# Kernel tuning notes

Hardware: AMD Instinct MI355X
Metric: run time of the kernel (lower is better)

Reference implementation:

```python
import jax, jax.numpy as jnp
import numpy as np

D_MODEL = 1024
N_HEADS = 16
D_K = D_MODEL // N_HEADS
MAX_SEQ = 2048
THETA = 10000.0


def _make_cos_sin():
    # cos_sin[i, k, 0] = cos(i / theta**(2k/d_k)), [.., 1] = sin(...)
    pos = np.arange(MAX_SEQ, dtype=np.float32)[:, None]
    k = np.arange(D_K // 2, dtype=np.float32)[None, :]
    ang = pos / (THETA ** (2.0 * k / D_K))
    return jnp.asarray(np.stack([np.cos(ang), np.sin(ang)], axis=-1), dtype=jnp.float32)


def setup_inputs() -> dict:
    key = jax.random.key(0)
    ks = jax.random.split(key, 5)
    std = 2.0 / (D_MODEL + D_MODEL)
    def w(k):
        return std * jax.random.truncated_normal(k, -3.0, 3.0, (D_MODEL, D_MODEL), dtype=jnp.float32)
    return {
        "x": jax.random.normal(ks[0], (4, 2048, D_MODEL), dtype=jnp.float32),
        "Wq": w(ks[1]),
        "Wk": w(ks[2]),
        "Wv": w(ks[3]),
        "Wo": w(ks[4]),
        "cos_sin": _make_cos_sin(),
        "token_positions": jnp.arange(2048, dtype=jnp.int32),
    }


def _rope(x, cos_sin, pos):
    # x: [B, H, S, d_k]; rotate consecutive pairs
    B, H, S, d = x.shape
    xt = x.reshape(B, H, S, d // 2, 2)
    cos = cos_sin[pos, :, 0]  # [S, d/2]
    sin = cos_sin[pos, :, 1]
    x0, x1 = xt[..., 0], xt[..., 1]
    r0 = cos * x0 - sin * x1
    r1 = sin * x0 + cos * x1
    return jnp.stack([r0, r1], axis=-1).reshape(B, H, S, d)


def reference(x, Wq, Wk, Wv, Wo, cos_sin, token_positions):
    B, S, D = x.shape
    H, d = N_HEADS, D_K
    def proj(W):
        y = jnp.einsum('bsi,oi->bso', x, W)
        return y.reshape(B, S, H, d).transpose(0, 2, 1, 3)  # [B,H,S,d]
    q = _rope(proj(Wq), cos_sin, token_positions)
    k = _rope(proj(Wk), cos_sin, token_positions)
    v = proj(Wv)
    scores = jnp.einsum('bhqd,bhkd->bhqk', q, k) / jnp.sqrt(jnp.float32(d))
    causal = jnp.tril(jnp.ones((S, S), dtype=bool))
    scores = jnp.where(causal, scores, -jnp.inf)
    attn = jax.nn.softmax(scores, axis=-1)
    out = jnp.einsum('bhqk,bhkd->bhqd', attn, v)
    out = out.transpose(0, 2, 1, 3).reshape(B, S, D)
    return jnp.einsum('bsi,oi->bso', out, Wo)
```

## Files before the change

kernel.cpp:

```cpp
#include <hip/hip_runtime.h>

constexpr int B_  = 4;
constexpr int S_  = 2048;
constexpr int D_  = 1024;
constexpr int H_  = 16;
constexpr int DK_ = 64;
constexpr int M_  = B_ * S_;

typedef __attribute__((ext_vector_type(8))) short short8;
typedef __attribute__((ext_vector_type(4))) float f32x4;
typedef __attribute__((ext_vector_type(4))) unsigned short us4;
typedef __attribute__((ext_vector_type(4))) unsigned int u32x4;

__device__ __forceinline__ unsigned short f2b(float f) {
  unsigned int u = __float_as_uint(f);
  u += 0x7FFFu + ((u >> 16) & 1u);
  return (unsigned short)(u >> 16);
}
__device__ __forceinline__ float b2f(unsigned short h) {
  return __uint_as_float(((unsigned int)h) << 16);
}
__device__ __forceinline__ unsigned int cvtpk(float lo, float hi) {
  unsigned int w;
  asm("v_cvt_pk_bf16_f32 %0, %1, %2" : "=v"(w) : "v"(lo), "v"(hi));
  return w;
}
__device__ __forceinline__ float exp2v(float x) {
  float r;
  asm("v_exp_f32 %0, %1" : "=v"(r) : "v"(x));
  return r;
}

#define GLOAD16(g, l) __builtin_amdgcn_global_load_lds( \
    (const __attribute__((address_space(1))) unsigned int*)(g), \
    (__attribute__((address_space(3))) unsigned int*)(l), 16, 0, 0)

__global__ __launch_bounds__(256) void conv_kernel(
    const float* __restrict__ x,
    const float* __restrict__ wq, const float* __restrict__ wk, const float* __restrict__ wv,
    unsigned short* __restrict__ xb, unsigned short* __restrict__ wb)
{
  const int NX4 = (M_ * D_) / 4;
  const int NW4 = (3 * D_ * D_) / 4;
  int stride = gridDim.x * blockDim.x;
  for (int i = blockIdx.x * blockDim.x + threadIdx.x; i < NX4 + NW4; i += stride) {
    const float4* src; unsigned short* dst; int o;
    if (i < NX4) { src = (const float4*)x; dst = xb; o = i; }
    else {
      int wi = i - NX4;
      int mat = wi >> 18;
      o = wi & 262143;
      src = (const float4*)(mat == 0 ? wq : (mat == 1 ? wk : wv));
      dst = wb + mat * (D_ * D_);
    }
    float4 v = src[o];
    us4 r; r.x = f2b(v.x); r.y = f2b(v.y); r.z = f2b(v.z); r.w = f2b(v.w);
    *(us4*)(dst + o * 4) = r;
  }
}

__global__ __launch_bounds__(256) void conv_wo_kernel(
    const float* __restrict__ wo, unsigned short* __restrict__ wob)
{
  int i = blockIdx.x * 256 + threadIdx.x;
  float4 v = ((const float4*)wo)[i];
  us4 r; r.x = f2b(v.x); r.y = f2b(v.y); r.z = f2b(v.z); r.w = f2b(v.w);
  *(us4*)(wob + i * 4) = r;
}

__global__ __launch_bounds__(256, 2) void gemm_qkv_kernel(
    const unsigned short* __restrict__ xb,
    const unsigned short* __restrict__ wb,
    const float* __restrict__ cs,
    const int* __restrict__ pos,
    unsigned short* __restrict__ qb,
    unsigned short* __restrict__ kb,
    unsigned short* __restrict__ vtb)
{
  __shared__ unsigned short As[2][128 * 64];
  __shared__ unsigned short Bs[2][128 * 64];
  const int tid  = threadIdx.x;
  const int lane = tid & 63;
  const int wid  = tid >> 6;
  const int wm = wid >> 1, wn = wid & 1;
  const int m0 = blockIdx.x * 128;
  const int n0 = blockIdx.y * 128;
  const int l15 = lane & 15, l4 = lane >> 4;
  const int swz7 = l15 & 7;

  int srow[4], sgcc[4], slds[4];
  #pragma unroll
  for (int j = 0; j < 4; ++j) {
    int c = tid + j * 256;
    srow[j] = c >> 3;
    int cc  = c & 7;
    sgcc[j] = cc ^ (srow[j] & 7);
    slds[j] = (wid * 64 + j * 256) * 8;
  }

  f32x4 acc[4][4] = {};

  #pragma unroll
  for (int j = 0; j < 4; ++j) {
    GLOAD16(xb + (m0 + srow[j]) * D_ + sgcc[j] * 8, &As[0][slds[j]]);
    GLOAD16(wb + (n0 + srow[j]) * D_ + sgcc[j] * 8, &Bs[0][slds[j]]);
  }
  __syncthreads();

  for (int t = 0; t < 16; ++t) {
    const int cur = t & 1, nxt = cur ^ 1;
    if (t < 15) {
      const int kcol = (t + 1) * 64;
      #pragma unroll
      for (int j = 0; j < 4; ++j) {
        GLOAD16(xb + (m0 + srow[j]) * D_ + kcol + sgcc[j] * 8, &As[nxt][slds[j]]);
        GLOAD16(wb + (n0 + srow[j]) * D_ + kcol + sgcc[j] * 8, &Bs[nxt][slds[j]]);
      }
    }
    const unsigned short* Ab = &As[cur][0];
    const unsigned short* Bb = &Bs[cur][0];
    #pragma unroll
    for (int ks = 0; ks < 2; ++ks) {
      const int cc = (ks * 4 + l4) ^ swz7;
      short8 af[4], bfr[4];
      #pragma unroll
      for (int mi = 0; mi < 4; ++mi) af[mi]  = *(const short8*)&Ab[(wm*64 + mi*16 + l15)*64 + cc*8];
      #pragma unroll
      for (int ni = 0; ni < 4; ++ni) bfr[ni] = *(const short8*)&Bb[(wn*64 + ni*16 + l15)*64 + cc*8];
      __builtin_amdgcn_s_setprio(1);
      #pragma unroll
      for (int mi = 0; mi < 4; ++mi)
        #pragma unroll
        for (int ni = 0; ni < 4; ++ni)
          acc[mi][ni] = __builtin_amdgcn_mfma_f32_16x16x32_bf16(af[mi], bfr[ni], acc[mi][ni], 0, 0, 0);
      __builtin_amdgcn_s_setprio(0);
    }
    __syncthreads();
  }

  const int bidx = m0 >> 11;
  const int sbase = (m0 & 2047) + wm * 64;

  if (n0 < 2048) {
    unsigned short* dst = (n0 < 1024) ? qb : kb;
    const int nn0 = n0 & 1023;
    const float2* cs2 = (const float2*)cs;
    const float sg = (l15 & 1) ? 1.0f : -1.0f;
    #pragma unroll
    for (int mi = 0; mi < 4; ++mi)
      #pragma unroll
      for (int j = 0; j < 4; ++j) {
        int s = sbase + mi*16 + l4*4 + j;
        int p = pos[s];
        #pragma unroll
        for (int ni = 0; ni < 4; ++ni) {
          int col = nn0 + wn*64 + ni*16 + l15;
          int h = col >> 6, dd = col & 63;
          float val = acc[mi][ni][j];
          float par = __shfl_xor(val, 1);
          float2 cv = cs2[p*32 + (dd >> 1)];
          float r = fmaf(cv.x, val, sg * cv.y * par);
          dst[((bidx*H_ + h)*S_ + s)*DK_ + dd] = f2b(r);
        }
      }
  } else {
    const int nn0 = n0 & 1023;
    const int hB = (nn0 + wn*64) >> 6;
    #pragma unroll
    for (int mi = 0; mi < 4; ++mi) {
      int s4 = sbase + mi*16 + l4*4;
      int a  = s4 >> 2, bgr = a & 7;
      int s4p = ((a & ~7) + ((bgr & 3)*2 + (bgr >> 2))) << 2;
      #pragma unroll
      for (int ni = 0; ni < 4; ++ni) {
        int dd = ni*16 + l15;
        uint2 w;
        w.x = cvtpk(acc[mi][ni][0], acc[mi][ni][1]);
        w.y = cvtpk(acc[mi][ni][2], acc[mi][ni][3]);
        *(uint2*)(vtb + ((bidx*H_ + hB)*DK_ + dd)*S_ + s4p) = w;
      }
    }
  }
}

__global__ __launch_bounds__(256, 4) void attn_kernel(
    const unsigned short* __restrict__ qb,
    const unsigned short* __restrict__ kb,
    const unsigned short* __restrict__ vtb,
    unsigned short* __restrict__ ao)
{
  __shared__ unsigned short Ks[2][64 * 64];
  __shared__ unsigned short Vs[2][64 * 64];
  const int tid = threadIdx.x, lane = tid & 63, wid = tid >> 6;
  const int l15 = lane & 15, l4 = lane >> 4;
  const int swz7 = l15 & 7;

  const int id  = blockIdx.x;
  const int xcd = id & 7, rem = id >> 3;
  const int bh  = xcd * 8 + (rem & 7);
  const int qt  = 15 - (rem >> 3);
  const int q0  = qt * 128;
  const int nkt = 2 * qt + 2;

  const unsigned short* qp = qb  + bh * S_ * DK_;
  const unsigned short* kp = kb  + bh * S_ * DK_;
  const unsigned short* vp = vtb + bh * DK_ * S_;
  const int bidx = bh >> 4, h = bh & 15;

  int srow[2], sgcc[2], slds[2];
  #pragma unroll
  for (int j = 0; j < 2; ++j) {
    int c = tid + j * 256;
    srow[j] = c >> 3;
    int cc  = c & 7;
    sgcc[j] = cc ^ (srow[j] & 7);
    slds[j] = (wid * 64 + j * 256) * 8;
  }

  const float QSC = 0.18033688f;
  short8 qf[2][2];
  #pragma unroll
  for (int y = 0; y < 2; ++y)
    #pragma unroll
    for (int kbk = 0; kbk < 2; ++kbk) {
      short8 raw = *(const short8*)(qp + (q0 + y*64 + wid*16 + l15)*DK_ + kbk*32 + l4*8);
      #pragma unroll
      for (int i = 0; i < 8; ++i) {
        float f = b2f((unsigned short)raw[i]) * QSC;
        raw[i] = (short)f2b(f);
      }
      qf[y][kbk] = raw;
    }

  f32x4 oacc[2][4] = {};
  float mrun[2] = {-1e30f, -1e30f}, lrun[2] = {0.0f, 0.0f};

  #pragma unroll
  for (int j = 0; j < 2; ++j) {
    GLOAD16(kp + srow[j]*DK_ + sgcc[j]*8, &Ks[0][slds[j]]);
    GLOAD16(vp + srow[j]*S_  + sgcc[j]*8, &Vs[0][slds[j]]);
  }
  __syncthreads();

  for (int kt = 0; kt < nkt; ++kt) {
    const int cur = kt & 1, nxt = cur ^ 1;
    if (kt + 1 < nkt) {
      const int kb0 = (kt + 1) * 64;
      #pragma unroll
      for (int j = 0; j < 2; ++j) {
        GLOAD16(kp + (kb0 + srow[j])*DK_ + sgcc[j]*8, &Ks[nxt][slds[j]]);
        GLOAD16(vp + srow[j]*S_ + kb0   + sgcc[j]*8, &Vs[nxt][slds[j]]);
      }
    }

    #pragma unroll
    for (int y = 0; y < 2; ++y) {
      if (kt > 2*qt + y) continue;

      f32x4 sc[4];
      __builtin_amdgcn_s_setprio(1);
      #pragma unroll
      for (int nb = 0; nb < 4; ++nb) {
        const int rb = (nb*16 + l15) * 64;
        short8 k0 = *(const short8*)&Ks[cur][rb + ((l4     ^ swz7) * 8)];
        short8 k1 = *(const short8*)&Ks[cur][rb + (((4+l4) ^ swz7) * 8)];
        f32x4 z = {};
        z = __builtin_amdgcn_mfma_f32_16x16x32_bf16(k0, qf[y][0], z, 0, 0, 0);
        z = __builtin_amdgcn_mfma_f32_16x16x32_bf16(k1, qf[y][1], z, 0, 0, 0);
        sc[nb] = z;
      }
      __builtin_amdgcn_s_setprio(0);

      if (kt == 2*qt + y) {
        const int qg = q0 + y*64 + wid*16 + l15;
        #pragma unroll
        for (int nb = 0; nb < 4; ++nb)
          #pragma unroll
          for (int j = 0; j < 4; ++j) {
            int kg = kt*64 + nb*16 + l4*4 + j;
            if (kg > qg) sc[nb][j] = -1e30f;
          }
      }

      float mq[4];
      #pragma unroll
      for (int nb = 0; nb < 4; ++nb)
        mq[nb] = fmaxf(fmaxf(sc[nb][0], sc[nb][1]), fmaxf(sc[nb][2], sc[nb][3]));
      float tm = fmaxf(fmaxf(mq[0], mq[1]), fmaxf(mq[2], mq[3]));
      tm = fmaxf(tm, __shfl_xor(tm, 16));
      tm = fmaxf(tm, __shfl_xor(tm, 32));
      if (!__all(tm - mrun[y] <= 8.0f)) {
        float mnew = fmaxf(mrun[y], tm);
        float corr = exp2v(mrun[y] - mnew);
        mrun[y] = mnew;
        lrun[y] *= corr;
        #pragma unroll
        for (int nb = 0; nb < 4; ++nb)
          #pragma unroll
          for (int j = 0; j < 4; ++j) oacc[y][nb][j] *= corr;
      }
      float sq[4];
      #pragma unroll
      for (int nb = 0; nb < 4; ++nb) {
        #pragma unroll
        for (int j = 0; j < 4; ++j) sc[nb][j] = exp2v(sc[nb][j] - mrun[y]);
        sq[nb] = (sc[nb][0] + sc[nb][1]) + (sc[nb][2] + sc[nb][3]);
      }
      float rs = (sq[0] + sq[1]) + (sq[2] + sq[3]);
      rs += __shfl_xor(rs, 16);
      rs += __shfl_xor(rs, 32);
      lrun[y] += rs;

      u32x4 pa0v = { cvtpk(sc[0][0], sc[0][1]), cvtpk(sc[0][2], sc[0][3]),
                     cvtpk(sc[1][0], sc[1][1]), cvtpk(sc[1][2], sc[1][3]) };
      u32x4 pa1v = { cvtpk(sc[2][0], sc[2][1]), cvtpk(sc[2][2], sc[2][3]),
                     cvtpk(sc[3][0], sc[3][1]), cvtpk(sc[3][2], sc[3][3]) };
      short8 pa0 = __builtin_bit_cast(short8, pa0v);
      short8 pa1 = __builtin_bit_cast(short8, pa1v);

      __builtin_amdgcn_s_setprio(1);
      #pragma unroll
      for (int nb = 0; nb < 4; ++nb) {
        const int rb = (nb*16 + l15) * 64;
        short8 v0 = *(const short8*)&Vs[cur][rb + ((l4     ^ swz7) * 8)];
        short8 v1 = *(const short8*)&Vs[cur][rb + (((4+l4) ^ swz7) * 8)];
        oacc[y][nb] = __builtin_amdgcn_mfma_f32_16x16x32_bf16(v0, pa0, oacc[y][nb], 0, 0, 0);
        oacc[y][nb] = __builtin_amdgcn_mfma_f32_16x16x32_bf16(v1, pa1, oacc[y][nb], 0, 0, 0);
      }
      __builtin_amdgcn_s_setprio(0);
    }

    __syncthreads();
  }

  #pragma unroll
  for (int y = 0; y < 2; ++y) {
    float inv = 1.0f / lrun[y];
    int row = q0 + y*64 + wid*16 + l15;
    unsigned short* obase = ao + ((bidx*S_ + row)*H_ + h)*DK_;
    #pragma unroll
    for (int nb = 0; nb < 4; ++nb) {
      uint2 w;
      w.x = cvtpk(oacc[y][nb][0] * inv, oacc[y][nb][1] * inv);
      w.y = cvtpk(oacc[y][nb][2] * inv, oacc[y][nb][3] * inv);
      *(uint2*)(obase + nb*16 + l4*4) = w;
    }
  }
}

__global__ __launch_bounds__(256, 2) void gemm_out_kernel(
    const unsigned short* __restrict__ ao,
    const unsigned short* __restrict__ wob,
    float* __restrict__ out)
{
  __shared__ unsigned short As[2][128 * 64];
  __shared__ unsigned short Bs[2][128 * 64];
  const int tid = threadIdx.x, lane = tid & 63, wid = tid >> 6;
  const int wm = wid >> 1, wn = wid & 1;
  const int m0 = blockIdx.x * 128, n0 = blockIdx.y * 128;
  const int l15 = lane & 15, l4 = lane >> 4;
  const int swz7 = l15 & 7;

  int srow[4], sgcc[4], slds[4];
  #pragma unroll
  for (int j = 0; j < 4; ++j) {
    int c = tid + j * 256;
    srow[j] = c >> 3;
    int cc  = c & 7;
    sgcc[j] = cc ^ (srow[j] & 7);
    slds[j] = (wid * 64 + j * 256) * 8;
  }

  f32x4 acc[4][4] = {};

  #pragma unroll
  for (int j = 0; j < 4; ++j) {
    GLOAD16(ao  + (m0 + srow[j]) * D_ + sgcc[j] * 8, &As[0][slds[j]]);
    GLOAD16(wob + (n0 + srow[j]) * D_ + sgcc[j] * 8, &Bs[0][slds[j]]);
  }
  __syncthreads();

  for (int t = 0; t < 16; ++t) {
    const int cur = t & 1, nxt = cur ^ 1;
    if (t < 15) {
      const int kcol = (t + 1) * 64;
      #pragma unroll
      for (int j = 0; j < 4; ++j) {
        GLOAD16(ao  + (m0 + srow[j]) * D_ + kcol + sgcc[j] * 8, &As[nxt][slds[j]]);
        GLOAD16(wob + (n0 + srow[j]) * D_ + kcol + sgcc[j] * 8, &Bs[nxt][slds[j]]);
      }
    }
    const unsigned short* Ab = &As[cur][0];
    const unsigned short* Bb = &Bs[cur][0];
    #pragma unroll
    for (int ks = 0; ks < 2; ++ks) {
      const int cc = (ks * 4 + l4) ^ swz7;
      short8 af[4], bfr[4];
      #pragma unroll
      for (int mi = 0; mi < 4; ++mi) af[mi]  = *(const short8*)&Ab[(wm*64 + mi*16 + l15)*64 + cc*8];
      #pragma unroll
      for (int ni = 0; ni < 4; ++ni) bfr[ni] = *(const short8*)&Bb[(wn*64 + ni*16 + l15)*64 + cc*8];
      __builtin_amdgcn_s_setprio(1);
      #pragma unroll
      for (int mi = 0; mi < 4; ++mi)
        #pragma unroll
        for (int ni = 0; ni < 4; ++ni)
          acc[mi][ni] = __builtin_amdgcn_mfma_f32_16x16x32_bf16(af[mi], bfr[ni], acc[mi][ni], 0, 0, 0);
      __builtin_amdgcn_s_setprio(0);
    }
    __syncthreads();
  }

  #pragma unroll
  for (int mi = 0; mi < 4; ++mi)
    #pragma unroll
    for (int ni = 0; ni < 4; ++ni)
      #pragma unroll
      for (int j = 0; j < 4; ++j) {
        int row = m0 + wm*64 + mi*16 + l4*4 + j;
        int col = n0 + wn*64 + ni*16 + l15;
        out[row * D_ + col] = acc[mi][ni][j];
      }
}

extern "C" void kernel_launch(void* const* d_in, const int* in_sizes, int n_in,
                              void* d_out, int out_size, void* d_ws, size_t ws_size,
                              hipStream_t stream)
{
  const float* x  = (const float*)d_in[0];
  const float* wq = (const float*)d_in[1];
  const float* wk = (const float*)d_in[2];
  const float* wv = (const float*)d_in[3];
  const float* wo = (const float*)d_in[4];
  const float* cs = (const float*)d_in[5];
  const int*  pos = (const int*)d_in[6];
  float* out = (float*)d_out;

  unsigned short* xb = (unsigned short*)d_out;
  unsigned short* wb = xb + M_ * D_;

  unsigned short* qb  = (unsigned short*)d_ws;
  unsigned short* kbf = qb  + M_ * D_;
  unsigned short* vtb = kbf + M_ * D_;
  unsigned short* aob = vtb + M_ * D_;
  unsigned short* wob = qb;

  conv_kernel<<<dim3(2048), dim3(256), 0, stream>>>(x, wq, wk, wv, xb, wb);
  gemm_qkv_kernel<<<dim3(64, 24), dim3(256), 0, stream>>>(xb, wb, cs, pos, qb, kbf, vtb);
  attn_kernel<<<dim3(1024), dim3(256), 0, stream>>>(qb, kbf, vtb, aob);
  conv_wo_kernel<<<dim3(1024), dim3(256), 0, stream>>>(wo, wob);
  gemm_out_kernel<<<dim3(64, 8), dim3(256), 0, stream>>>(aob, wob, out);

  (void)in_sizes; (void)n_in; (void)out_size; (void)ws_size;
}
```

Measured before the change: 173.6 us.

## Replace double-buffered K=64 GEMM pipeline with single-buffer K=32 tiles

Both projection GEMMs drop the double-buffered 64-wide K staging and use a single 32-wide K tile per iteration, with two barriers around each load and a new XOR swizzle for the narrower rows. This quarters LDS use per block, which may allow more resident blocks, and simplifies the loop. The cost is that loads no longer overlap with MFMA work inside a block, and the barrier count per K element doubles.

Measured after the change: 181.4 us. 1.04x slower.

```diff
diff --git a/kernel.cpp b/kernel.cpp
--- a/kernel.cpp
+++ b/kernel.cpp
@@ -77,8 +77,8 @@
     unsigned short* __restrict__ kb,
     unsigned short* __restrict__ vtb)
 {
-  __shared__ unsigned short As[2][128 * 64];
-  __shared__ unsigned short Bs[2][128 * 64];
+  __shared__ unsigned short As[128 * 32];
+  __shared__ unsigned short Bs[128 * 32];
   const int tid  = threadIdx.x;
   const int lane = tid & 63;
   const int wid  = tid >> 6;
@@ -86,56 +86,42 @@
   const int m0 = blockIdx.x * 128;
   const int n0 = blockIdx.y * 128;
   const int l15 = lane & 15, l4 = lane >> 4;
-  const int swz7 = l15 & 7;
-
-  int srow[4], sgcc[4], slds[4];
-  #pragma unroll
-  for (int j = 0; j < 4; ++j) {
+  const int fsw = (l15 >> 1) & 3;
+
+  int srow[2], sgcc[2], slds[2];
+  #pragma unroll
+  for (int j = 0; j < 2; ++j) {
     int c = tid + j * 256;
-    srow[j] = c >> 3;
-    int cc  = c & 7;
-    sgcc[j] = cc ^ (srow[j] & 7);
+    srow[j] = c >> 2;
+    int cc  = c & 3;
+    sgcc[j] = cc ^ ((srow[j] >> 1) & 3);
     slds[j] = (wid * 64 + j * 256) * 8;
   }
 
   f32x4 acc[4][4] = {};
 
-  #pragma unroll
-  for (int j = 0; j < 4; ++j) {
-    GLOAD16(xb + (m0 + srow[j]) * D_ + sgcc[j] * 8, &As[0][slds[j]]);
-    GLOAD16(wb + (n0 + srow[j]) * D_ + sgcc[j] * 8, &Bs[0][slds[j]]);
-  }
-  __syncthreads();
-
-  for (int t = 0; t < 16; ++t) {
-    const int cur = t & 1, nxt = cur ^ 1;
-    if (t < 15) {
-      const int kcol = (t + 1) * 64;
-      #pragma unroll
-      for (int j = 0; j < 4; ++j) {
-        GLOAD16(xb + (m0 + srow[j]) * D_ + kcol + sgcc[j] * 8, &As[nxt][slds[j]]);
-        GLOAD16(wb + (n0 + srow[j]) * D_ + kcol + sgcc[j] * 8, &Bs[nxt][slds[j]]);
-      }
-    }
-    const unsigned short* Ab = &As[cur][0];
-    const unsigned short* Bb = &Bs[cur][0];
-    #pragma unroll
-    for (int ks = 0; ks < 2; ++ks) {
-      const int cc = (ks * 4 + l4) ^ swz7;
-      short8 af[4], bfr[4];
-      #pragma unroll
-      for (int mi = 0; mi < 4; ++mi) af[mi]  = *(const short8*)&Ab[(wm*64 + mi*16 + l15)*64 + cc*8];
-      #pragma unroll
-      for (int ni = 0; ni < 4; ++ni) bfr[ni] = *(const short8*)&Bb[(wn*64 + ni*16 + l15)*64 + cc*8];
-      __builtin_amdgcn_s_setprio(1);
-      #pragma unroll
-      for (int mi = 0; mi < 4; ++mi)
-        #pragma unroll
-        for (int ni = 0; ni < 4; ++ni)
-          acc[mi][ni] = __builtin_amdgcn_mfma_f32_16x16x32_bf16(af[mi], bfr[ni], acc[mi][ni], 0, 0, 0);
-      __builtin_amdgcn_s_setprio(0);
-    }
+  for (int t = 0; t < 32; ++t) {
     __syncthreads();
+    GLOAD16(xb + (m0 + srow[0]) * D_ + t*32 + sgcc[0]*8, &As[slds[0]]);
+    GLOAD16(xb + (m0 + srow[1]) * D_ + t*32 + sgcc[1]*8, &As[slds[1]]);
+    GLOAD16(wb + (n0 + srow[0]) * D_ + t*32 + sgcc[0]*8, &Bs[slds[0]]);
+    GLOAD16(wb + (n0 + srow[1]) * D_ + t*32 + sgcc[1]*8, &Bs[slds[1]]);
+    __syncthreads();
+
+    short8 af[4], bfr[4];
+    #pragma unroll
+    for (int mi = 0; mi < 4; ++mi)
+      af[mi]  = *(const short8*)&As[(wm*64 + mi*16 + l15)*32 + ((l4 ^ fsw)*8)];
+    #pragma unroll
+    for (int ni = 0; ni < 4; ++ni)
+      bfr[ni] = *(const short8*)&Bs[(wn*64 + ni*16 + l15)*32 + ((l4 ^ fsw)*8)];
+    __builtin_amdgcn_s_setprio(1);
+    #pragma unroll
+    for (int mi = 0; mi < 4; ++mi)
+      #pragma unroll
+      for (int ni = 0; ni < 4; ++ni)
+        acc[mi][ni] = __builtin_amdgcn_mfma_f32_16x16x32_bf16(af[mi], bfr[ni], acc[mi][ni], 0, 0, 0);
+    __builtin_amdgcn_s_setprio(0);
   }
 
   const int bidx = m0 >> 11;
@@ -353,62 +339,48 @@
     const unsigned short* __restrict__ wob,
     float* __restrict__ out)
 {
-  __shared__ unsigned short As[2][128 * 64];
-  __shared__ unsigned short Bs[2][128 * 64];
+  __shared__ unsigned short As[128 * 32];
+  __shared__ unsigned short Bs[128 * 32];
   const int tid = threadIdx.x, lane = tid & 63, wid = tid >> 6;
   const int wm = wid >> 1, wn = wid & 1;
   const int m0 = blockIdx.x * 128, n0 = blockIdx.y * 128;
   const int l15 = lane & 15, l4 = lane >> 4;
-  const int swz7 = l15 & 7;
-
-  int srow[4], sgcc[4], slds[4];
-  #pragma unroll
-  for (int j = 0; j < 4; ++j) {
+  const int fsw = (l15 >> 1) & 3;
+
+  int srow[2], sgcc[2], slds[2];
+  #pragma unroll
+  for (int j = 0; j < 2; ++j) {
     int c = tid + j * 256;
-    srow[j] = c >> 3;
-    int cc  = c & 7;
-    sgcc[j] = cc ^ (srow[j] & 7);
+    srow[j] = c >> 2;
+    int cc  = c & 3;
+    sgcc[j] = cc ^ ((srow[j] >> 1) & 3);
     slds[j] = (wid * 64 + j * 256) * 8;
   }
 
   f32x4 acc[4][4] = {};
 
-  #pragma unroll
-  for (int j = 0; j < 4; ++j) {
-    GLOAD16(ao  + (m0 + srow[j]) * D_ + sgcc[j] * 8, &As[0][slds[j]]);
-    GLOAD16(wob + (n0 + srow[j]) * D_ + sgcc[j] * 8, &Bs[0][slds[j]]);
-  }
-  __syncthreads();
-
-  for (int t = 0; t < 16; ++t) {
-    const int cur = t & 1, nxt = cur ^ 1;
-    if (t < 15) {
-      const int kcol = (t + 1) * 64;
-      #pragma unroll
-      for (int j = 0; j < 4; ++j) {
-        GLOAD16(ao  + (m0 + srow[j]) * D_ + kcol + sgcc[j] * 8, &As[nxt][slds[j]]);
-        GLOAD16(wob + (n0 + srow[j]) * D_ + kcol + sgcc[j] * 8, &Bs[nxt][slds[j]]);
-      }
-    }
-    const unsigned short* Ab = &As[cur][0];
-    const unsigned short* Bb = &Bs[cur][0];
-    #pragma unroll
-    for (int ks = 0; ks < 2; ++ks) {
-      const int cc = (ks * 4 + l4) ^ swz7;
-      short8 af[4], bfr[4];
-      #pragma unroll
-      for (int mi = 0; mi < 4; ++mi) af[mi]  = *(const short8*)&Ab[(wm*64 + mi*16 + l15)*64 + cc*8];
-      #pragma unroll
-      for (int ni = 0; ni < 4; ++ni) bfr[ni] = *(const short8*)&Bb[(wn*64 + ni*16 + l15)*64 + cc*8];
-      __builtin_amdgcn_s_setprio(1);
-      #pragma unroll
-      for (int mi = 0; mi < 4; ++mi)
-        #pragma unroll
-        for (int ni = 0; ni < 4; ++ni)
-          acc[mi][ni] = __builtin_amdgcn_mfma_f32_16x16x32_bf16(af[mi], bfr[ni], acc[mi][ni], 0, 0, 0);
-      __builtin_amdgcn_s_setprio(0);
-    }
+  for (int t = 0; t < 32; ++t) {
     __syncthreads();
+    GLOAD16(ao  + (m0 + srow[0]) * D_ + t*32 + sgcc[0]*8, &As[slds[0]]);
+    GLOAD16(ao  + (m0 + srow[1]) * D_ + t*32 + sgcc[1]*8, &As[slds[1]]);
+    GLOAD16(wob + (n0 + srow[0]) * D_ + t*32 + sgcc[0]*8, &Bs[slds[0]]);
+    GLOAD16(wob + (n0 + srow[1]) * D_ + t*32 + sgcc[1]*8, &Bs[slds[1]]);
+    __syncthreads();
+
+    short8 af[4], bfr[4];
+    #pragma unroll
+    for (int mi = 0; mi < 4; ++mi)
+      af[mi]  = *(const short8*)&As[(wm*64 + mi*16 + l15)*32 + ((l4 ^ fsw)*8)];
+    #pragma unroll
+    for (int ni = 0; ni < 4; ++ni)
+      bfr[ni] = *(const short8*)&Bs[(wn*64 + ni*16 + l15)*32 + ((l4 ^ fsw)*8)];
+    __builtin_amdgcn_s_setprio(1);
+    #pragma unroll
+    for (int mi = 0; mi < 4; ++mi)
+      #pragma unroll
+      for (int ni = 0; ni < 4; ++ni)
+        acc[mi][ni] = __builtin_amdgcn_mfma_f32_16x16x32_bf16(af[mi], bfr[ni], acc[mi][ni], 0, 0, 0);
+    __builtin_amdgcn_s_setprio(0);
   }
 
   #pragma unroll
```
